# Performance work log

Measured on AMD Instinct MI355X. Metric: run time of the kernel, lower is better.

Reference implementation:

```python
import jax, jax.numpy as jnp
import numpy as np

N_NODES = 50000
N_EDGES = 800000
HIDDEN = 128


def setup_inputs() -> dict:
    key = jax.random.key(0)
    k_emb, k_ei, k1, k2, k3, kb1, kb2, kb3 = jax.random.split(key, 8)
    emb = jax.random.normal(k_emb, (N_NODES, HIDDEN), dtype=jnp.float32)
    edge_index = jax.random.randint(k_ei, (2, N_EDGES), 0, N_NODES, dtype=jnp.int64)
    h = HIDDEN
    # MLP([2h, 4h, h, 1]) weights, Kaiming-uniform-ish init
    def lin(k, fan_in, fan_out):
        bound = 1.0 / np.sqrt(fan_in)
        return jax.random.uniform(k, (fan_in, fan_out), jnp.float32, -bound, bound)
    W1 = lin(k1, 2 * h, 4 * h)
    b1 = jax.random.uniform(kb1, (4 * h,), jnp.float32, -1.0 / np.sqrt(2 * h), 1.0 / np.sqrt(2 * h))
    W2 = lin(k2, 4 * h, h)
    b2 = jax.random.uniform(kb2, (h,), jnp.float32, -1.0 / np.sqrt(4 * h), 1.0 / np.sqrt(4 * h))
    W3 = lin(k3, h, 1)
    b3 = jax.random.uniform(kb3, (1,), jnp.float32, -1.0 / np.sqrt(h), 1.0 / np.sqrt(h))
    return {"emb": emb, "edge_index": edge_index,
            "W1": W1, "b1": b1, "W2": W2, "b2": b2, "W3": W3, "b3": b3}


def reference(emb, edge_index, W1, b1, W2, b2, W3, b3):
    # learn_edge_att=True path: gather endpoints, concat, 3-layer MLP
    col, row = edge_index[0], edge_index[1]
    f12 = jnp.concatenate([emb[col], emb[row]], axis=-1)  # [E, 2h]
    x = jax.nn.relu(f12 @ W1 + b1)                         # [E, 4h]
    x = jax.nn.relu(x @ W2 + b2)                           # [E, h]
    att_log_logits = x @ W3 + b3                           # [E, 1]
    return att_log_logits
```

## Files before the change

### kernel.cpp

```cpp
#include <hip/hip_runtime.h>
#include <hip/hip_bf16.h>
#include <stdint.h>

#define N_EDGES   800000
#define N_NODESC  50000
#define HID       128

typedef __attribute__((ext_vector_type(8))) short bf16x8;
typedef __attribute__((ext_vector_type(4))) short bf16x4;
typedef __attribute__((ext_vector_type(4))) float f32x4;

__device__ __forceinline__ short f2bf(float f) {
    union { float f; uint32_t u; } v; v.f = f;
    uint32_t r = v.u + 0x7FFFu + ((v.u >> 16) & 1u);
    return (short)(r >> 16);
}
__device__ __forceinline__ float bf2f(short s) {
    union { uint32_t u; float f; } v;
    v.u = ((uint32_t)(uint16_t)s) << 16;
    return v.f;
}

#define PQ_OFF   0UL
#define W1S_OFF  102400000UL
#define W2S_OFF  (W1S_OFF + 262144UL)

__global__ __launch_bounds__(256) void swizzle_kernel(const float* __restrict__ W1,
                                                      const float* __restrict__ W2,
                                                      short* __restrict__ W1s,
                                                      short* __restrict__ W2s) {
    int t = blockIdx.x * 256 + threadIdx.x;
    int lane = t & 63;
    int kq = lane >> 4;
    int nn = lane & 15;
    if (t < 16384) {
        int frag = t >> 6;
        int kc = frag >> 6;
        int nt = frag & 63;
        int n = nt * 16 + nn;
        int kbase = kc * 32 + kq * 8;
        bf16x8 v;
        #pragma unroll
        for (int j = 0; j < 8; ++j) {
            int k = kbase + j;
            float f = (n < 512) ? W1[k * 512 + n] : W1[(128 + k) * 512 + (n - 512)];
            v[j] = f2bf(f);
        }
        *(bf16x8*)(W1s + frag * 512 + lane * 8) = v;
    } else if (t < 24576) {
        int t2 = t - 16384;
        int frag = t2 >> 6;
        int kc = frag >> 3;
        int nt = frag & 7;
        int n = nt * 16 + nn;
        int kbase = kc * 32 + kq * 8;
        bf16x8 v;
        #pragma unroll
        for (int j = 0; j < 8; ++j) v[j] = f2bf(W2[(kbase + j) * HID + n]);
        *(bf16x8*)(W2s + frag * 512 + lane * 8) = v;
    }
}

__global__ __launch_bounds__(256) void precompute_kernel(const float* __restrict__ emb,
                                                         const short* __restrict__ W1s,
                                                         short* __restrict__ PQ) {
    __shared__ short ldsA[4][16][136];
    int lane = threadIdx.x & 63;
    int w = threadIdx.x >> 6;
    int nb = blockIdx.x * 16;

    const float* src = emb + (size_t)nb * 128;
    #pragma unroll
    for (int q = 0; q < 8; ++q) {
        int flat = q * 256 + lane * 4;
        f32x4 v = *(const f32x4*)(src + flat);
        int r = flat >> 7, c = flat & 127;
        bf16x4 b;
        b[0] = f2bf(v[0]); b[1] = f2bf(v[1]); b[2] = f2bf(v[2]); b[3] = f2bf(v[3]);
        *(bf16x4*)(&ldsA[w][r][c]) = b;
    }

    f32x4 acc[16];
    #pragma unroll
    for (int i = 0; i < 16; ++i) acc[i] = (f32x4){0.f, 0.f, 0.f, 0.f};

    int m = lane & 15;
    int kq = lane >> 4;
    for (int kc = 0; kc < 4; ++kc) {
        bf16x8 a = *(const bf16x8*)(&ldsA[w][m][kc * 32 + kq * 8]);
        #pragma unroll
        for (int nt = 0; nt < 16; ++nt) {
            int frag = kc * 64 + (w * 16 + nt);
            bf16x8 b = *(const bf16x8*)(W1s + frag * 512 + lane * 8);
            acc[nt] = __builtin_amdgcn_mfma_f32_16x16x32_bf16(a, b, acc[nt], 0, 0, 0);
        }
    }

    #pragma unroll
    for (int nt = 0; nt < 16; ++nt) {
        #pragma unroll
        for (int r = 0; r < 4; ++r) {
            int node = nb + kq * 4 + r;
            int n = w * 256 + nt * 16 + m;
            PQ[(size_t)node * 1024 + n] = f2bf(acc[nt][r]);
        }
    }
}

__global__ __launch_bounds__(256) void edge_kernel(const short* __restrict__ PQ,
                                                   const int* __restrict__ ei,
                                                   const float* __restrict__ b1,
                                                   const short* __restrict__ W2s,
                                                   const float* __restrict__ b2,
                                                   const float* __restrict__ W3,
                                                   const float* __restrict__ b3,
                                                   float* __restrict__ out) {
    __shared__ short x1[4][16][520];
    int lane = threadIdx.x & 63;
    int w = threadIdx.x >> 6;
    int e0 = blockIdx.x * 64 + w * 16;

    f32x4 b1a = *(const f32x4*)(b1 + lane * 8);
    f32x4 b1b = *(const f32x4*)(b1 + lane * 8 + 4);

    int idx0 = 0;
    if (lane < 32) idx0 = ei[(lane >> 4) * N_EDGES + e0 + (lane & 15)];

    #pragma unroll 4
    for (int i = 0; i < 16; ++i) {
        int ce = __shfl(idx0, i, 64);
        int re = __shfl(idx0, 16 + i, 64);
        bf16x8 p = *(const bf16x8*)(PQ + (size_t)ce * 1024 + lane * 8);
        bf16x8 q = *(const bf16x8*)(PQ + (size_t)re * 1024 + 512 + lane * 8);
        bf16x8 s;
        #pragma unroll
        for (int j = 0; j < 8; ++j) {
            float f = bf2f(p[j]) + bf2f(q[j]) + (j < 4 ? b1a[j] : b1b[j - 4]);
            f = f > 0.f ? f : 0.f;
            s[j] = f2bf(f);
        }
        *(bf16x8*)(&x1[w][i][lane * 8]) = s;
    }

    f32x4 acc[8];
    #pragma unroll
    for (int nt = 0; nt < 8; ++nt) acc[nt] = (f32x4){0.f, 0.f, 0.f, 0.f};
    int m = lane & 15;
    int kq = lane >> 4;
    for (int kc = 0; kc < 16; ++kc) {
        bf16x8 a = *(const bf16x8*)(&x1[w][m][kc * 32 + kq * 8]);
        #pragma unroll
        for (int nt = 0; nt < 8; ++nt) {
            bf16x8 b = *(const bf16x8*)(W2s + (kc * 8 + nt) * 512 + lane * 8);
            acc[nt] = __builtin_amdgcn_mfma_f32_16x16x32_bf16(a, b, acc[nt], 0, 0, 0);
        }
    }

    float b2v[8], w3v[8];
    #pragma unroll
    for (int nt = 0; nt < 8; ++nt) {
        b2v[nt] = b2[nt * 16 + m];
        w3v[nt] = W3[nt * 16 + m];
    }
    float b3s = b3[0];
    float partial[4] = {0.f, 0.f, 0.f, 0.f};
    #pragma unroll
    for (int nt = 0; nt < 8; ++nt) {
        #pragma unroll
        for (int r = 0; r < 4; ++r) {
            float x2 = acc[nt][r] + b2v[nt];
            x2 = x2 > 0.f ? x2 : 0.f;
            partial[r] += x2 * w3v[nt];
        }
    }
    #pragma unroll
    for (int r = 0; r < 4; ++r) {
        #pragma unroll
        for (int off = 1; off < 16; off <<= 1)
            partial[r] += __shfl_xor(partial[r], off, 64);
        if (m == 0) out[e0 + kq * 4 + r] = partial[r] + b3s;
    }
}

extern "C" void kernel_launch(void* const* d_in, const int* in_sizes, int n_in,
                              void* d_out, int out_size, void* d_ws, size_t ws_size,
                              hipStream_t stream) {
    const float* emb = (const float*)d_in[0];
    const int*   ei  = (const int*)d_in[1];
    const float* W1  = (const float*)d_in[2];
    const float* b1  = (const float*)d_in[3];
    const float* W2  = (const float*)d_in[4];
    const float* b2  = (const float*)d_in[5];
    const float* W3  = (const float*)d_in[6];
    const float* b3  = (const float*)d_in[7];
    float* out = (float*)d_out;

    short* PQ  = (short*)((char*)d_ws + PQ_OFF);
    short* W1s = (short*)((char*)d_ws + W1S_OFF);
    short* W2s = (short*)((char*)d_ws + W2S_OFF);

    swizzle_kernel<<<96, 256, 0, stream>>>(W1, W2, W1s, W2s);
    precompute_kernel<<<N_NODESC / 16, 256, 0, stream>>>(emb, W1s, PQ);
    edge_kernel<<<N_EDGES / 64, 256, 0, stream>>>(PQ, ei, b1, W2s, b2, W3, b3, out);
}
```

Before: 467.0 us.

## Gather edge features directly into MFMA operands and reuse W2 fragments across tiles

```diff
diff --git a/kernel.cpp b/kernel.cpp
--- a/kernel.cpp
+++ b/kernel.cpp
@@ -63,31 +63,26 @@
 
 __global__ __launch_bounds__(256) void precompute_kernel(const float* __restrict__ emb,
                                                          const short* __restrict__ W1s,
+                                                         const float* __restrict__ b1,
                                                          short* __restrict__ PQ) {
-    __shared__ short ldsA[4][16][136];
     int lane = threadIdx.x & 63;
     int w = threadIdx.x >> 6;
     int nb = blockIdx.x * 16;
-
-    const float* src = emb + (size_t)nb * 128;
-    #pragma unroll
-    for (int q = 0; q < 8; ++q) {
-        int flat = q * 256 + lane * 4;
-        f32x4 v = *(const f32x4*)(src + flat);
-        int r = flat >> 7, c = flat & 127;
-        bf16x4 b;
-        b[0] = f2bf(v[0]); b[1] = f2bf(v[1]); b[2] = f2bf(v[2]); b[3] = f2bf(v[3]);
-        *(bf16x4*)(&ldsA[w][r][c]) = b;
-    }
-
-    f32x4 acc[16];
-    #pragma unroll
-    for (int i = 0; i < 16; ++i) acc[i] = (f32x4){0.f, 0.f, 0.f, 0.f};
-
     int m = lane & 15;
     int kq = lane >> 4;
+
+    f32x4 acc[16];
+    #pragma unroll
+    for (int i = 0; i < 16; ++i) acc[i] = (f32x4){0.f, 0.f, 0.f, 0.f};
+
+    const float* arow = emb + (size_t)(nb + m) * 128 + kq * 8;
+    #pragma unroll
     for (int kc = 0; kc < 4; ++kc) {
-        bf16x8 a = *(const bf16x8*)(&ldsA[w][m][kc * 32 + kq * 8]);
+        f32x4 a0 = *(const f32x4*)(arow + kc * 32);
+        f32x4 a1 = *(const f32x4*)(arow + kc * 32 + 4);
+        bf16x8 a;
+        a[0] = f2bf(a0[0]); a[1] = f2bf(a0[1]); a[2] = f2bf(a0[2]); a[3] = f2bf(a0[3]);
+        a[4] = f2bf(a1[0]); a[5] = f2bf(a1[1]); a[6] = f2bf(a1[2]); a[7] = f2bf(a1[3]);
         #pragma unroll
         for (int nt = 0; nt < 16; ++nt) {
             int frag = kc * 64 + (w * 16 + nt);
@@ -98,61 +93,68 @@
 
     #pragma unroll
     for (int nt = 0; nt < 16; ++nt) {
+        int n = w * 256 + nt * 16 + m;
+        float bias = (n < 512) ? b1[n] : 0.0f;
         #pragma unroll
         for (int r = 0; r < 4; ++r) {
             int node = nb + kq * 4 + r;
-            int n = w * 256 + nt * 16 + m;
-            PQ[(size_t)node * 1024 + n] = f2bf(acc[nt][r]);
-        }
-    }
-}
-
-__global__ __launch_bounds__(256) void edge_kernel(const short* __restrict__ PQ,
-                                                   const int* __restrict__ ei,
-                                                   const float* __restrict__ b1,
-                                                   const short* __restrict__ W2s,
-                                                   const float* __restrict__ b2,
-                                                   const float* __restrict__ W3,
-                                                   const float* __restrict__ b3,
-                                                   float* __restrict__ out) {
-    __shared__ short x1[4][16][520];
+            PQ[(size_t)node * 1024 + n] = f2bf(acc[nt][r] + bias);
+        }
+    }
+}
+
+__global__ __launch_bounds__(256, 2) void edge_kernel(const short* __restrict__ PQ,
+                                                      const int* __restrict__ ei,
+                                                      const short* __restrict__ W2s,
+                                                      const float* __restrict__ b2,
+                                                      const float* __restrict__ W3,
+                                                      const float* __restrict__ b3,
+                                                      float* __restrict__ out) {
     int lane = threadIdx.x & 63;
     int w = threadIdx.x >> 6;
-    int e0 = blockIdx.x * 64 + w * 16;
-
-    f32x4 b1a = *(const f32x4*)(b1 + lane * 8);
-    f32x4 b1b = *(const f32x4*)(b1 + lane * 8 + 4);
-
-    int idx0 = 0;
-    if (lane < 32) idx0 = ei[(lane >> 4) * N_EDGES + e0 + (lane & 15)];
-
-    #pragma unroll 4
-    for (int i = 0; i < 16; ++i) {
-        int ce = __shfl(idx0, i, 64);
-        int re = __shfl(idx0, 16 + i, 64);
-        bf16x8 p = *(const bf16x8*)(PQ + (size_t)ce * 1024 + lane * 8);
-        bf16x8 q = *(const bf16x8*)(PQ + (size_t)re * 1024 + 512 + lane * 8);
-        bf16x8 s;
-        #pragma unroll
-        for (int j = 0; j < 8; ++j) {
-            float f = bf2f(p[j]) + bf2f(q[j]) + (j < 4 ? b1a[j] : b1b[j - 4]);
-            f = f > 0.f ? f : 0.f;
-            s[j] = f2bf(f);
-        }
-        *(bf16x8*)(&x1[w][i][lane * 8]) = s;
-    }
-
-    f32x4 acc[8];
-    #pragma unroll
-    for (int nt = 0; nt < 8; ++nt) acc[nt] = (f32x4){0.f, 0.f, 0.f, 0.f};
+    int e0 = blockIdx.x * 256 + w * 64;
     int m = lane & 15;
     int kq = lane >> 4;
+
+    int idx_c = ei[e0 + lane];
+    int idx_r = ei[N_EDGES + e0 + lane];
+
+    const short* pb[4];
+    const short* qb[4];
+    #pragma unroll
+    for (int t = 0; t < 4; ++t) {
+        int ce = __shfl(idx_c, t * 16 + m, 64);
+        int re = __shfl(idx_r, t * 16 + m, 64);
+        pb[t] = PQ + (size_t)ce * 1024 + kq * 8;
+        qb[t] = PQ + (size_t)re * 1024 + 512 + kq * 8;
+    }
+
+    f32x4 acc[4][8];
+    #pragma unroll
+    for (int t = 0; t < 4; ++t)
+        #pragma unroll
+        for (int nt = 0; nt < 8; ++nt) acc[t][nt] = (f32x4){0.f, 0.f, 0.f, 0.f};
+
+    #pragma unroll 1
     for (int kc = 0; kc < 16; ++kc) {
-        bf16x8 a = *(const bf16x8*)(&x1[w][m][kc * 32 + kq * 8]);
-        #pragma unroll
-        for (int nt = 0; nt < 8; ++nt) {
-            bf16x8 b = *(const bf16x8*)(W2s + (kc * 8 + nt) * 512 + lane * 8);
-            acc[nt] = __builtin_amdgcn_mfma_f32_16x16x32_bf16(a, b, acc[nt], 0, 0, 0);
+        bf16x8 b[8];
+        #pragma unroll
+        for (int nt = 0; nt < 8; ++nt)
+            b[nt] = *(const bf16x8*)(W2s + (kc * 8 + nt) * 512 + lane * 8);
+        #pragma unroll
+        for (int t = 0; t < 4; ++t) {
+            bf16x8 p = *(const bf16x8*)(pb[t] + kc * 32);
+            bf16x8 q = *(const bf16x8*)(qb[t] + kc * 32);
+            bf16x8 a;
+            #pragma unroll
+            for (int j = 0; j < 8; ++j) {
+                float f = bf2f(p[j]) + bf2f(q[j]);
+                f = f > 0.f ? f : 0.f;
+                a[j] = f2bf(f);
+            }
+            #pragma unroll
+            for (int nt = 0; nt < 8; ++nt)
+                acc[t][nt] = __builtin_amdgcn_mfma_f32_16x16x32_bf16(a, b[nt], acc[t][nt], 0, 0, 0);
         }
     }
 
@@ -163,22 +165,25 @@
         w3v[nt] = W3[nt * 16 + m];
     }
     float b3s = b3[0];
-    float partial[4] = {0.f, 0.f, 0.f, 0.f};
-    #pragma unroll
-    for (int nt = 0; nt < 8; ++nt) {
+    #pragma unroll
+    for (int t = 0; t < 4; ++t) {
+        float partial[4] = {0.f, 0.f, 0.f, 0.f};
+        #pragma unroll
+        for (int nt = 0; nt < 8; ++nt) {
+            #pragma unroll
+            for (int r = 0; r < 4; ++r) {
+                float x2 = acc[t][nt][r] + b2v[nt];
+                x2 = x2 > 0.f ? x2 : 0.f;
+                partial[r] += x2 * w3v[nt];
+            }
+        }
         #pragma unroll
         for (int r = 0; r < 4; ++r) {
-            float x2 = acc[nt][r] + b2v[nt];
-            x2 = x2 > 0.f ? x2 : 0.f;
-            partial[r] += x2 * w3v[nt];
-        }
-    }
-    #pragma unroll
-    for (int r = 0; r < 4; ++r) {
-        #pragma unroll
-        for (int off = 1; off < 16; off <<= 1)
-            partial[r] += __shfl_xor(partial[r], off, 64);
-        if (m == 0) out[e0 + kq * 4 + r] = partial[r] + b3s;
+            #pragma unroll
+            for (int off = 1; off < 16; off <<= 1)
+                partial[r] += __shfl_xor(partial[r], off, 64);
+            if (m == 0) out[e0 + t * 16 + kq * 4 + r] = partial[r] + b3s;
+        }
     }
 }
 
@@ -200,6 +205,6 @@
     short* W2s = (short*)((char*)d_ws + W2S_OFF);
 
     swizzle_kernel<<<96, 256, 0, stream>>>(W1, W2, W1s, W2s);
-    precompute_kernel<<<N_NODESC / 16, 256, 0, stream>>>(emb, W1s, PQ);
-    edge_kernel<<<N_EDGES / 64, 256, 0, stream>>>(PQ, ei, b1, W2s, b2, W3, b3, out);
-}
+    precompute_kernel<<<N_NODESC / 16, 256, 0, stream>>>(emb, W1s, b1, PQ);
+    edge_kernel<<<N_EDGES / 256, 256, 0, stream>>>(PQ, ei, W2s, b2, W3, b3, out);
+}
```

Result: faster. 430.6 us (-7.8%).
